# Kernel optimization log

Hardware: AMD Instinct MI355X
Metric: run time of the kernel (lower is better)

## Reference

```python
import jax, jax.numpy as jnp
import numpy as np

B, LATENT, P, NUM_ATOMS, H, L, E = 16, 128, 16, 64, 64, 4, 32768
N = P * NUM_ATOMS  # 1024

def _lin(k, i, o, s=0.05):
    kw, kb = jax.random.split(k)
    return jax.random.normal(kw, (i, o), jnp.float32) * s, jax.random.normal(kb, (o,), jnp.float32) * s

def setup_inputs() -> dict:
    key = jax.random.key(0)
    ks = jax.random.split(key, 32)
    z = jax.random.normal(ks[0], (B, LATENT), jnp.float32)
    edge_index = jax.random.randint(ks[1], (2, E), 0, N, jnp.int32)
    # build_node_features: (frame/P, atom/num_atoms, 1) per node
    fr = jnp.repeat(jnp.arange(P), NUM_ATOMS) / P
    at = jnp.tile(jnp.arange(NUM_ATOMS), P) / NUM_ATOMS
    node_features = jnp.stack([fr, at, jnp.ones(N)], -1).astype(jnp.float32)
    Wg, bg = _lin(ks[2], LATENT, H)
    Wn, bn = _lin(ks[3], 3, H)
    def stack(fn, base):
        outs = [fn(jax.random.fold_in(key, base + l)) for l in range(L)]
        return tuple(jnp.stack(t) for t in zip(*outs))
    eW1, eb1 = stack(lambda k: _lin(k, 2 * H + 1, H), 100)
    eW2, eb2 = stack(lambda k: _lin(k, H, H), 200)
    cW1, cb1 = stack(lambda k: _lin(k, H, H), 300)
    cW2 = jnp.stack([jax.random.normal(jax.random.fold_in(key, 400 + l), (H, 1), jnp.float32) * 0.05 for l in range(L)])
    nW1, nb1 = stack(lambda k: _lin(k, 2 * H, H), 500)
    nW2, nb2 = stack(lambda k: _lin(k, H, H), 600)
    lng = jnp.ones((L, H), jnp.float32)
    lnb = jnp.zeros((L, H), jnp.float32)
    oW1, ob1 = _lin(ks[4], H, H)
    oW2, ob2 = _lin(ks[5], H, 3)
    return dict(z=z, edge_index=edge_index, node_features=node_features, Wg=Wg, bg=bg, Wn=Wn, bn=bn,
                eW1=eW1, eb1=eb1, eW2=eW2, eb2=eb2, cW1=cW1, cb1=cb1, cW2=cW2,
                nW1=nW1, nb1=nb1, nW2=nW2, nb2=nb2, lng=lng, lnb=lnb,
                oW1=oW1, ob1=ob1, oW2=oW2, ob2=ob2)

def _forward(z, edge_index, node_features, Wg, bg, Wn, bn, eW1, eb1, eW2, eb2,
             cW1, cb1, cW2, nW1, nb1, nW2, nb2, lng, lnb, oW1, ob1, oW2, ob2):
    b = z.shape[0]
    n = node_features.shape[0]
    row, col = edge_index[0], edge_index[1]  # aggregate messages to row
    counts = jnp.clip(jnp.zeros((n,), jnp.float32).at[row].add(1.0), 1.0, None)
    g = z @ Wg + bg                              # [B,H]
    h = (node_features @ Wn + bn)[None] + g[:, None]  # [B,N,H]
    pos = jnp.zeros((b, n, 3), h.dtype)
    for l in range(L):
        hi, hj = h[:, row], h[:, col]            # [B,E,H] gathers
        diff = pos[:, row] - pos[:, col]         # [B,E,3]
        d2 = jnp.sum(diff * diff, -1, keepdims=True)
        m = jax.nn.silu(jnp.concatenate([hi, hj, d2], -1) @ eW1[l] + eb1[l])
        m = jax.nn.silu(m @ eW2[l] + eb2[l])     # [B,E,H]
        w = jax.nn.silu(m @ cW1[l] + cb1[l]) @ cW2[l]  # [B,E,1]
        trans = diff * w
        pos = pos + jnp.zeros_like(pos).at[:, row].add(trans) / counts[None, :, None]
        agg = jnp.zeros_like(h).at[:, row].add(m)      # scatter-sum to nodes
        u = jax.nn.silu(jnp.concatenate([h, agg], -1) @ nW1[l] + nb1[l]) @ nW2[l] + nb2[l]
        h = h + u                                 # node residual
        mu = jnp.mean(h, -1, keepdims=True)
        var = jnp.mean((h - mu) ** 2, -1, keepdims=True)
        h = (h - mu) * jax.lax.rsqrt(var + 1e-5) * lng[l] + lnb[l]
    out = jax.nn.relu(h @ oW1 + ob1) @ oW2 + ob2   # [B,N,3]
    return out.reshape(b, -1)

def reference(z, edge_index, node_features, Wg, bg, Wn, bn, eW1, eb1, eW2, eb2,
              cW1, cb1, cW2, nW1, nb1, nW2, nb2, lng, lnb, oW1, ob1, oW2, ob2):
    return _forward(z, edge_index, node_features, Wg, bg, Wn, bn, eW1, eb1, eW2, eb2,
                    cW1, cb1, cW2, nW1, nb1, nW2, nb2, lng, lnb, oW1, ob1, oW2, ob2)
```

## Files before the change

### kernel.cpp

```cpp
#include <hip/hip_runtime.h>
#include <hip/hip_bf16.h>


namespace {

constexpr int kB = 16, kN = 1024, kH = 64, kE = 32768, kLat = 128;
constexpr int kC = 24;
constexpr int kMaxItems = 2560;

typedef __attribute__((ext_vector_type(8))) short short8;
typedef __attribute__((ext_vector_type(4))) float floatx4;

__device__ __forceinline__ unsigned short f2bf(float f){
  union { float f; unsigned int u; } v; v.f = f;
  unsigned int r = v.u + 0x7fffu + ((v.u >> 16) & 1u);
  return (unsigned short)(r >> 16);
}
__device__ __forceinline__ unsigned int packbf(float a, float b){
  return ((unsigned int)f2bf(b) << 16) | (unsigned int)f2bf(a);
}
__device__ __forceinline__ unsigned int pack2f(float a, float b){
  unsigned int ua = __float_as_uint(a) + 0x8000u;
  unsigned int ub = __float_as_uint(b) + 0x8000u;
  return __builtin_amdgcn_perm(ub, ua, 0x07060302);
}
__device__ __forceinline__ float bflo(unsigned int u){
  union { unsigned int u; float f; } v; v.u = u << 16; return v.f;
}
__device__ __forceinline__ float bfhi(unsigned int u){
  union { unsigned int u; float f; } v; v.u = u & 0xffff0000u; return v.f;
}
__device__ __forceinline__ float silu2(float x){
  float u = __builtin_amdgcn_exp2f(-1.44269504f * x);
  return x * __builtin_amdgcn_rcpf(1.0f + u);
}

__global__ void k_count(const int* ei, int* cntI){
  int e = blockIdx.x*256 + threadIdx.x;
  atomicAdd(&cntI[ei[e]], 1);
}

__global__ void k_scan(const int* cntI, int* off, int* ioff, int* fill,
                       int* items, int* nitems){
  __shared__ int s0[1024];
  __shared__ int s1[1024];
  int t = threadIdx.x;
  int c = cntI[t];
  s0[t] = c; __syncthreads();
  int* src = s0; int* dst = s1;
  for (int o = 1; o < 1024; o <<= 1){
    int v = src[t] + ((t >= o) ? src[t-o] : 0);
    dst[t] = v; __syncthreads();
    int* tmp = src; src = dst; dst = tmp;
  }
  int inc = src[t];
  off[t] = inc - c;
  if (t == 1023) off[1024] = inc;
  fill[t] = 0;
  int ic = (c + (kC-1)) / kC;
  __syncthreads();
  s0[t] = ic; __syncthreads();
  src = s0; dst = s1;
  for (int o = 1; o < 1024; o <<= 1){
    int v = src[t] + ((t >= o) ? src[t-o] : 0);
    dst[t] = v; __syncthreads();
    int* tmp = src; src = dst; dst = tmp;
  }
  int inc2 = src[t];
  int ib = inc2 - ic;
  ioff[t] = ib;
  if (t == 1023){ ioff[1024] = inc2; *nitems = inc2; }
  for (int s = 0; s < ic; s++) items[ib + s] = (t << 12) | s;
}

__global__ void k_bucket(const int* ei, const int* off, int* fill, int* ecol,
                         const float* eW2, unsigned short* wfragE,
                         const float* z, const float* Wg, const float* bg,
                         float* g){
  int e = blockIdx.x*256 + threadIdx.x;
  int r = ei[e];
  int s = atomicAdd(&fill[r], 1);
  ecol[off[r] + s] = ei[kE + e];
  if (blockIdx.x < 4){
    int l = blockIdx.x;
    for (int i = threadIdx.x; i < 4096; i += 256){
      int f = i >> 9, lane = (i >> 3) & 63, j8 = i & 7;
      int jt = f >> 1, ks = f & 1;
      int k = ks*32 + (lane >> 4)*8 + j8;
      int j = jt*16 + (lane & 15);
      wfragE[l*4096 + i] = f2bf(eW2[l*4096 + k*64 + j]);
    }
  } else if (blockIdx.x < 8){
    int b = (blockIdx.x - 4)*4 + (threadIdx.x >> 6);
    int j = threadIdx.x & 63;
    float acc = bg[j];
    for (int k = 0; k < kLat; k++) acc += z[b*kLat + k] * Wg[k*64 + j];
    g[b*64 + j] = acc;
  }
}

__device__ __forceinline__ void stage16k(float* Wl, const float* src, int tid){
  const float4* p = (const float4*)src;
  float4* d = (float4*)Wl;
  d[tid]       = p[tid];
  d[tid + 256] = p[tid + 256];
  d[tid + 512] = p[tid + 512];
  d[tid + 768] = p[tid + 768];
}
__device__ __forceinline__ void xtwrite(float* XTl, int j0, int r0,
                                        const float v[4][4]){
  #pragma unroll
  for (int j = 0; j < 4; j++){
    float4 t = { v[0][j], v[1][j], v[2][j], v[3][j] };
    *(float4*)(XTl + (j0 + j)*68 + r0) = t;
  }
}
__device__ __forceinline__ void gemm64(const float* Wl, const float* XTl,
                                       int j0, int r0, float acc[4][4]){
  #pragma unroll 4
  for (int k = 0; k < 64; k++){
    float4 w = *(const float4*)(Wl + k*64 + j0);
    float4 x = *(const float4*)(XTl + k*68 + r0);
    float xv[4] = { x.x, x.y, x.z, x.w };
    float wv[4] = { w.x, w.y, w.z, w.w };
    #pragma unroll
    for (int i = 0; i < 4; i++)
      #pragma unroll
      for (int j = 0; j < 4; j++)
        acc[i][j] += xv[i]*wv[j];
  }
}

__global__ __launch_bounds__(256, 1) void k_preA(const float* nf, const float* Wn,
      const float* bn, const float* g, const float* eW1, const float* eb1,
      float* An1, float* An2, float* Ag1, float* Ag2){
  __shared__ __align__(16) float W0[4096];
  __shared__ __align__(16) float W1[4096];
  __shared__ __align__(16) float HR[16*68];
  int tid = threadIdx.x;
  if (blockIdx.x == 64){
    int bb = tid >> 4, j0 = (tid & 15)*4;
    float a1[4] = {0.f,0.f,0.f,0.f}, a2[4] = {0.f,0.f,0.f,0.f};
    for (int k = 0; k < 64; k++){
      float gk = g[bb*64 + k];
      float4 w1 = *(const float4*)(eW1 + k*64 + j0);
      float4 w2 = *(const float4*)(eW1 + 4096 + k*64 + j0);
      a1[0] += gk*w1.x; a1[1] += gk*w1.y; a1[2] += gk*w1.z; a1[3] += gk*w1.w;
      a2[0] += gk*w2.x; a2[1] += gk*w2.y; a2[2] += gk*w2.z; a2[3] += gk*w2.w;
    }
    float4 o1 = { a1[0], a1[1], a1[2], a1[3] };
    float4 o2 = { a2[0], a2[1], a2[2], a2[3] };
    *(float4*)(Ag1 + bb*64 + j0) = o1;
    *(float4*)(Ag2 + bb*64 + j0) = o2;
    return;
  }
  {
    const float4* e1a = (const float4*)(eW1);
    const float4* e1b = (const float4*)(eW1 + 4096);
    for (int i = tid; i < 1024; i += 256){
      ((float4*)W0)[i] = e1a[i]; ((float4*)W1)[i] = e1b[i];
    }
  }
  int rl = tid >> 4, c = tid & 15, j0 = c*4;
  int n = blockIdx.x*16 + rl;
  float f0 = nf[n*3], f1 = nf[n*3+1], f2 = nf[n*3+2];
  float4 hv;
  hv.x = f0*Wn[j0+0] + f1*Wn[64+j0+0] + f2*Wn[128+j0+0] + bn[j0+0];
  hv.y = f0*Wn[j0+1] + f1*Wn[64+j0+1] + f2*Wn[128+j0+1] + bn[j0+1];
  hv.z = f0*Wn[j0+2] + f1*Wn[64+j0+2] + f2*Wn[128+j0+2] + bn[j0+2];
  hv.w = f0*Wn[j0+3] + f1*Wn[64+j0+3] + f2*Wn[128+j0+3] + bn[j0+3];
  *(float4*)(HR + rl*68 + j0) = hv;
  __syncthreads();
  float4 b1 = *(const float4*)(eb1 + j0);
  float a1[4] = { b1.x, b1.y, b1.z, b1.w };
  float a2[4] = { 0.f, 0.f, 0.f, 0.f };
  #pragma unroll 8
  for (int k = 0; k < 64; k++){
    float hk = HR[rl*68 + k];
    float4 w1 = *(const float4*)(W0 + k*64 + j0);
    float4 w2 = *(const float4*)(W1 + k*64 + j0);
    a1[0] += hk*w1.x; a1[1] += hk*w1.y; a1[2] += hk*w1.z; a1[3] += hk*w1.w;
    a2[0] += hk*w2.x; a2[1] += hk*w2.y; a2[2] += hk*w2.z; a2[3] += hk*w2.w;
  }
  float4 o1 = { a1[0], a1[1], a1[2], a1[3] };
  float4 o2 = { a2[0], a2[1], a2[2], a2[3] };
  *(float4*)(An1 + n*64 + j0) = o1;
  *(float4*)(An2 + n*64 + j0) = o2;
}

__global__ __launch_bounds__(256, 1) void k_pre1(const float* nf, const float* Wn,
      const float* bn, const float* g, const float* An1, const float* An2,
      const float* Ag1, const float* Ag2, float* h, float* A1t,
      unsigned short* A2bf){
  int idx = blockIdx.x*256 + threadIdx.x;
  int row = idx >> 4;
  int j0  = (idx & 15) * 4;
  int n = row >> 4, bb = row & 15;
  float4 a1 = *(const float4*)(An1 + n*64 + j0);
  float4 g1 = *(const float4*)(Ag1 + bb*64 + j0);
  a1.x += g1.x; a1.y += g1.y; a1.z += g1.z; a1.w += g1.w;
  *(float4*)(A1t + row*64 + j0) = a1;
  float4 a2 = *(const float4*)(An2 + n*64 + j0);
  float4 g2 = *(const float4*)(Ag2 + bb*64 + j0);
  a2.x += g2.x; a2.y += g2.y; a2.z += g2.z; a2.w += g2.w;
  uint2 pk; pk.x = packbf(a2.x, a2.y); pk.y = packbf(a2.z, a2.w);
  *(uint2*)(A2bf + row*64 + j0) = pk;
  float f0 = nf[n*3], f1 = nf[n*3+1], f2 = nf[n*3+2];
  float4 w0 = *(const float4*)(Wn + j0);
  float4 w1 = *(const float4*)(Wn + 64 + j0);
  float4 w2 = *(const float4*)(Wn + 128 + j0);
  float4 bv = *(const float4*)(bn + j0);
  float4 gv = *(const float4*)(g + bb*64 + j0);
  float4 hv;
  hv.x = f0*w0.x + f1*w1.x + f2*w2.x + bv.x + gv.x;
  hv.y = f0*w0.y + f1*w1.y + f2*w2.y + bv.y + gv.y;
  hv.z = f0*w0.z + f1*w1.z + f2*w2.z + bv.z + gv.z;
  hv.w = f0*w0.w + f1*w1.w + f2*w2.w + bv.w + gv.w;
  *(float4*)(h + (bb*1024 + n)*64 + j0) = hv;
}

__global__ __launch_bounds__(256, 3) void k_edge(const float* A1t,
      const unsigned short* A2bf, const unsigned short* wfragE,
      const float* eb2, int l, const int* off, const int* ecol,
      const int* items, const int* nitems, float* P){
  int w = blockIdx.x*4 + (threadIdx.x >> 6);
  if (w >= *nitems) return;
  int lane = threadIdx.x & 63;
  int m = lane & 15, quad = lane >> 4;
  int it = items[w];
  int r = it >> 12, s = it & 4095;
  int e0 = off[r] + s*kC;
  int e1 = min(off[r+1], e0 + kC);

  short8 wf[8];
  #pragma unroll
  for (int f = 0; f < 8; f++)
    wf[f] = *(const short8*)(wfragE + l*4096 + f*512 + lane*8);

  float4 a1[4];
  #pragma unroll
  for (int ks = 0; ks < 2; ks++){
    a1[ks*2+0] = *(const float4*)(A1t + (r<<10) + (m<<6) + ks*32 + quad*8);
    a1[ks*2+1] = *(const float4*)(A1t + (r<<10) + (m<<6) + ks*32 + quad*8 + 4);
  }
  floatx4 dini[4];
  #pragma unroll
  for (int jt = 0; jt < 4; jt++)
    dini[jt] = *(const floatx4*)(eb2 + l*64 + jt*16 + quad*4);
  floatx4 agg[4];
  #pragma unroll
  for (int jt = 0; jt < 4; jt++) agg[jt] = (floatx4){0.f,0.f,0.f,0.f};

  int c0 = ecol[e0];
  uint4 p0 = *(const uint4*)(A2bf + ((c0<<4)+m)*64 + quad*8);
  uint4 p1 = *(const uint4*)(A2bf + ((c0<<4)+m)*64 + 32 + quad*8);

  for (int e = e0; e < e1; e++){
    uint4 c_0 = p0, c_1 = p1;
    if (e + 1 < e1){
      int cn = ecol[e+1];
      p0 = *(const uint4*)(A2bf + ((cn<<4)+m)*64 + quad*8);
      p1 = *(const uint4*)(A2bf + ((cn<<4)+m)*64 + 32 + quad*8);
    }
    short8 bfr[2];
    #pragma unroll
    for (int ks = 0; ks < 2; ks++){
      uint4 a2r = (ks == 0) ? c_0 : c_1;
      float4 x0 = a1[ks*2+0];
      float4 x1 = a1[ks*2+1];
      float v0 = silu2(x0.x + bflo(a2r.x));
      float v1 = silu2(x0.y + bfhi(a2r.x));
      float v2 = silu2(x0.z + bflo(a2r.y));
      float v3 = silu2(x0.w + bfhi(a2r.y));
      float v4 = silu2(x1.x + bflo(a2r.z));
      float v5 = silu2(x1.y + bfhi(a2r.z));
      float v6 = silu2(x1.z + bflo(a2r.w));
      float v7 = silu2(x1.w + bfhi(a2r.w));
      union { uint4 u; short8 s; } bu;
      bu.u.x = pack2f(v0, v1); bu.u.y = pack2f(v2, v3);
      bu.u.z = pack2f(v4, v5); bu.u.w = pack2f(v6, v7);
      bfr[ks] = bu.s;
    }
    #pragma unroll
    for (int jt = 0; jt < 4; jt++){
      floatx4 d = dini[jt];
      d = __builtin_amdgcn_mfma_f32_16x16x32_bf16(wf[jt*2+0], bfr[0], d, 0, 0, 0);
      d = __builtin_amdgcn_mfma_f32_16x16x32_bf16(wf[jt*2+1], bfr[1], d, 0, 0, 0);
      floatx4 a = agg[jt];
      a.x += silu2(d.x); a.y += silu2(d.y);
      a.z += silu2(d.z); a.w += silu2(d.w);
      agg[jt] = a;
    }
  }
  #pragma unroll
  for (int jt = 0; jt < 4; jt++)
    *(floatx4*)(P + w*1024 + m*64 + jt*16 + quad*4) = agg[jt];
}

template <bool LAST>
__global__ __launch_bounds__(256, 1) void k_post(int l, float* h, const float* P,
      const int* ioff, const float* nW1, const float* nb1_, const float* nW2,
      const float* nb2_, const float* lng_, const float* lnb_,
      const float* eW1, const float* eb1_, float* A1t, unsigned short* A2bf,
      const float* oW1, const float* ob1_, const float* oW2, const float* ob2_,
      float* out){
  __shared__ __align__(16) float W[4096];
  __shared__ __align__(16) float XT[64*68];
  int tid = threadIdx.x;
  int bb = blockIdx.x >> 4;
  int n0 = (blockIdx.x & 15) * 64;
  int c = tid & 15, g = tid >> 4;
  int j0 = c*4, r0 = g*4;
  int rowbase = bb*1024 + n0 + r0;

  stage16k(W, nW1 + l*8192, tid);
  float hold[4][4];
  #pragma unroll
  for (int i = 0; i < 4; i++){
    float4 v = *(const float4*)(h + (rowbase + i)*64 + j0);
    hold[i][0]=v.x; hold[i][1]=v.y; hold[i][2]=v.z; hold[i][3]=v.w;
  }
  xtwrite(XT, j0, r0, hold);
  float acc[4][4];
  {
    float4 b1 = *(const float4*)(nb1_ + l*64 + j0);
    float bv[4] = { b1.x, b1.y, b1.z, b1.w };
    #pragma unroll
    for (int i = 0; i < 4; i++)
      #pragma unroll
      for (int j = 0; j < 4; j++) acc[i][j] = bv[j];
  }
  __syncthreads();
  gemm64(W, XT, j0, r0, acc);
  __syncthreads();

  stage16k(W, nW1 + l*8192 + 4096, tid);
  {
    float agt[4][4];
    #pragma unroll
    for (int i = 0; i < 4; i++){
      int n = n0 + r0 + i;
      float4 s = { 0.f, 0.f, 0.f, 0.f };
      int i0 = ioff[n], i1 = ioff[n+1];
      for (int it = i0; it < i1; it++){
        float4 v = *(const float4*)(P + it*1024 + bb*64 + j0);
        s.x += v.x; s.y += v.y; s.z += v.z; s.w += v.w;
      }
      agt[i][0]=s.x; agt[i][1]=s.y; agt[i][2]=s.z; agt[i][3]=s.w;
    }
    xtwrite(XT, j0, r0, agt);
  }
  __syncthreads();
  gemm64(W, XT, j0, r0, acc);
  #pragma unroll
  for (int i = 0; i < 4; i++)
    #pragma unroll
    for (int j = 0; j < 4; j++) acc[i][j] = silu2(acc[i][j]);
  __syncthreads();

  stage16k(W, nW2 + l*4096, tid);
  xtwrite(XT, j0, r0, acc);
  float u[4][4];
  {
    float4 b2 = *(const float4*)(nb2_ + l*64 + j0);
    float bv[4] = { b2.x, b2.y, b2.z, b2.w };
    #pragma unroll
    for (int i = 0; i < 4; i++)
      #pragma unroll
      for (int j = 0; j < 4; j++) u[i][j] = bv[j];
  }
  __syncthreads();
  gemm64(W, XT, j0, r0, u);
  float4 lgv = *(const float4*)(lng_ + l*64 + j0);
  float4 lbv = *(const float4*)(lnb_ + l*64 + j0);
  float hn[4][4];
  #pragma unroll
  for (int i = 0; i < 4; i++){
    float hv[4];
    #pragma unroll
    for (int j = 0; j < 4; j++) hv[j] = hold[i][j] + u[i][j];
    float s1 = hv[0]+hv[1]+hv[2]+hv[3];
    float s2 = hv[0]*hv[0]+hv[1]*hv[1]+hv[2]*hv[2]+hv[3]*hv[3];
    s1 += __shfl_xor(s1, 1, 64); s1 += __shfl_xor(s1, 2, 64);
    s1 += __shfl_xor(s1, 4, 64); s1 += __shfl_xor(s1, 8, 64);
    s2 += __shfl_xor(s2, 1, 64); s2 += __shfl_xor(s2, 2, 64);
    s2 += __shfl_xor(s2, 4, 64); s2 += __shfl_xor(s2, 8, 64);
    float mu  = s1 * (1.0f/64.0f);
    float var = s2 * (1.0f/64.0f) - mu*mu;
    float rs  = rsqrtf(var + 1e-5f);
    hn[i][0] = (hv[0]-mu)*rs*lgv.x + lbv.x;
    hn[i][1] = (hv[1]-mu)*rs*lgv.y + lbv.y;
    hn[i][2] = (hv[2]-mu)*rs*lgv.z + lbv.z;
    hn[i][3] = (hv[3]-mu)*rs*lgv.w + lbv.w;
  }

  if (!LAST){
    #pragma unroll
    for (int i = 0; i < 4; i++){
      float4 v = { hn[i][0], hn[i][1], hn[i][2], hn[i][3] };
      *(float4*)(h + (rowbase + i)*64 + j0) = v;
    }
    __syncthreads();
    stage16k(W, eW1 + (l+1)*8256, tid);
    xtwrite(XT, j0, r0, hn);
    float a1[4][4];
    {
      float4 b1 = *(const float4*)(eb1_ + (l+1)*64 + j0);
      float bv[4] = { b1.x, b1.y, b1.z, b1.w };
      #pragma unroll
      for (int i = 0; i < 4; i++)
        #pragma unroll
        for (int j = 0; j < 4; j++) a1[i][j] = bv[j];
    }
    __syncthreads();
    gemm64(W, XT, j0, r0, a1);
    __syncthreads();
    stage16k(W, eW1 + (l+1)*8256 + 4096, tid);
    float a2[4][4];
    #pragma unroll
    for (int i = 0; i < 4; i++)
      #pragma unroll
      for (int j = 0; j < 4; j++) a2[i][j] = 0.f;
    __syncthreads();
    gemm64(W, XT, j0, r0, a2);
    #pragma unroll
    for (int i = 0; i < 4; i++){
      int tb = ((n0 + r0 + i)*16 + bb)*64 + j0;
      float4 o1 = { a1[i][0], a1[i][1], a1[i][2], a1[i][3] };
      *(float4*)(A1t + tb) = o1;
      uint2 pk; pk.x = packbf(a2[i][0], a2[i][1]);
      pk.y = packbf(a2[i][2], a2[i][3]);
      *(uint2*)(A2bf + tb) = pk;
    }
  } else {
    __syncthreads();
    stage16k(W, oW1, tid);
    xtwrite(XT, j0, r0, hn);
    float tr[4][4];
    {
      float4 b1 = *(const float4*)(ob1_ + j0);
      float bv[4] = { b1.x, b1.y, b1.z, b1.w };
      #pragma unroll
      for (int i = 0; i < 4; i++)
        #pragma unroll
        for (int j = 0; j < 4; j++) tr[i][j] = bv[j];
    }
    __syncthreads();
    gemm64(W, XT, j0, r0, tr);
    #pragma unroll
    for (int i = 0; i < 4; i++)
      #pragma unroll
      for (int j = 0; j < 4; j++) tr[i][j] = fmaxf(tr[i][j], 0.f);
    float po[4][3];
    #pragma unroll
    for (int i = 0; i < 4; i++){ po[i][0]=0.f; po[i][1]=0.f; po[i][2]=0.f; }
    #pragma unroll
    for (int j = 0; j < 4; j++){
      float w0 = oW2[(j0+j)*3 + 0];
      float w1 = oW2[(j0+j)*3 + 1];
      float w2 = oW2[(j0+j)*3 + 2];
      #pragma unroll
      for (int i = 0; i < 4; i++){
        po[i][0] += tr[i][j]*w0;
        po[i][1] += tr[i][j]*w1;
        po[i][2] += tr[i][j]*w2;
      }
    }
    #pragma unroll
    for (int i = 0; i < 4; i++)
      #pragma unroll
      for (int uu = 0; uu < 3; uu++){
        float v = po[i][uu];
        v += __shfl_xor(v, 1, 64); v += __shfl_xor(v, 2, 64);
        v += __shfl_xor(v, 4, 64); v += __shfl_xor(v, 8, 64);
        po[i][uu] = v;
      }
    if (c == 0){
      #pragma unroll
      for (int i = 0; i < 4; i++){
        int n = n0 + r0 + i;
        out[bb*3072 + n*3 + 0] = po[i][0] + ob2_[0];
        out[bb*3072 + n*3 + 1] = po[i][1] + ob2_[1];
        out[bb*3072 + n*3 + 2] = po[i][2] + ob2_[2];
      }
    }
  }
}

}

extern "C" void kernel_launch(void* const* d_in, const int* in_sizes, int n_in,
                              void* d_out, int out_size, void* d_ws, size_t ws_size,
                              hipStream_t stream){
  const float* z   = (const float*)d_in[0];
  const int*   ei  = (const int*)d_in[1];
  const float* nf  = (const float*)d_in[2];
  const float* Wg  = (const float*)d_in[3];  const float* bg  = (const float*)d_in[4];
  const float* Wn  = (const float*)d_in[5];  const float* bn  = (const float*)d_in[6];
  const float* eW1 = (const float*)d_in[7];  const float* eb1 = (const float*)d_in[8];
  const float* eW2 = (const float*)d_in[9];  const float* eb2 = (const float*)d_in[10];
  const float* nW1 = (const float*)d_in[14]; const float* nb1 = (const float*)d_in[15];
  const float* nW2 = (const float*)d_in[16]; const float* nb2 = (const float*)d_in[17];
  const float* lng = (const float*)d_in[18]; const float* lnb = (const float*)d_in[19];
  const float* oW1 = (const float*)d_in[20]; const float* ob1 = (const float*)d_in[21];
  const float* oW2 = (const float*)d_in[22]; const float* ob2 = (const float*)d_in[23];

  float* W      = (float*)d_ws;
  float* h      = W;
  float* A1t    = W + 1048576;
  unsigned short* A2bf   = (unsigned short*)(W + 2097152);
  unsigned short* wfragE = (unsigned short*)(W + 2621440);
  float* P      = W + 2629632;
  float* g      = W + 5251072;
  int*   cntI   = (int*)(W + 5252096);
  int*   off    = cntI + 1024;
  int*   ioff   = off + 1025;
  int*   fill   = ioff + 1025;
  int*   items  = fill + 1024;
  int*   nitems = items + 2560;
  int*   ecol   = nitems + 1;
  float* An1    = W + 5291776;
  float* An2    = An1 + 65536;
  float* Ag1    = An2 + 65536;
  float* Ag2    = Ag1 + 1024;

  hipMemsetAsync(cntI, 0, 1024*sizeof(int), stream);
  k_count <<<128, 256, 0, stream>>>(ei, cntI);
  k_scan  <<<1,  1024, 0, stream>>>(cntI, off, ioff, fill, items, nitems);
  k_bucket<<<128, 256, 0, stream>>>(ei, off, fill, ecol, eW2, wfragE, z, Wg, bg, g);
  k_preA  <<<65,  256, 0, stream>>>(nf, Wn, bn, g, eW1, eb1, An1, An2, Ag1, Ag2);
  k_pre1  <<<1024,256, 0, stream>>>(nf, Wn, bn, g, An1, An2, Ag1, Ag2, h, A1t, A2bf);

  for (int l = 0; l < 4; l++){
    k_edge<<<640, 256, 0, stream>>>(A1t, A2bf, wfragE, eb2, l, off, ecol,
                                    items, nitems, P);
    if (l < 3)
      k_post<false><<<256, 256, 0, stream>>>(l, h, P, ioff, nW1, nb1, nW2, nb2,
            lng, lnb, eW1, eb1, A1t, A2bf, oW1, ob1, oW2, ob2, (float*)d_out);
    else
      k_post<true> <<<256, 256, 0, stream>>>(l, h, P, ioff, nW1, nb1, nW2, nb2,
            lng, lnb, eW1, eb1, A1t, A2bf, oW1, ob1, oW2, ob2, (float*)d_out);
  }
}
```

Baseline: 356.7 us.

## Fuse edge message pass into per-node layer kernel with ping-pong buffers

```diff
diff --git a/kernel.cpp b/kernel.cpp
--- a/kernel.cpp
+++ b/kernel.cpp
@@ -4,9 +4,7 @@
 
 namespace {
 
-constexpr int kB = 16, kN = 1024, kH = 64, kE = 32768, kLat = 128;
-constexpr int kC = 24;
-constexpr int kMaxItems = 2560;
+constexpr int kE = 32768, kLat = 128;
 
 typedef __attribute__((ext_vector_type(8))) short short8;
 typedef __attribute__((ext_vector_type(4))) float floatx4;
@@ -35,18 +33,48 @@
   return x * __builtin_amdgcn_rcpf(1.0f + u);
 }
 
-__global__ void k_count(const int* ei, int* cntI){
-  int e = blockIdx.x*256 + threadIdx.x;
-  atomicAdd(&cntI[ei[e]], 1);
-}
-
-__global__ void k_scan(const int* cntI, int* off, int* ioff, int* fill,
-                       int* items, int* nitems){
+__device__ __forceinline__ void stage16k(float* Wl, const float* src, int tid){
+  const float4* p = (const float4*)src;
+  float4* d = (float4*)Wl;
+  d[tid]       = p[tid];
+  d[tid + 256] = p[tid + 256];
+  d[tid + 512] = p[tid + 512];
+  d[tid + 768] = p[tid + 768];
+}
+__device__ __forceinline__ void xtwrite(float* XTl, int j0, int r0,
+                                        const float v[4][4]){
+  #pragma unroll
+  for (int j = 0; j < 4; j++){
+    float4 t = { v[0][j], v[1][j], v[2][j], v[3][j] };
+    *(float4*)(XTl + (j0 + j)*68 + r0) = t;
+  }
+}
+__device__ __forceinline__ void gemm64(const float* Wl, const float* XTl,
+                                       int j0, int r0, float acc[4][4]){
+  #pragma unroll 4
+  for (int k = 0; k < 64; k++){
+    float4 w = *(const float4*)(Wl + k*64 + j0);
+    float4 x = *(const float4*)(XTl + k*68 + r0);
+    float xv[4] = { x.x, x.y, x.z, x.w };
+    float wv[4] = { w.x, w.y, w.z, w.w };
+    #pragma unroll
+    for (int i = 0; i < 4; i++)
+      #pragma unroll
+      for (int j = 0; j < 4; j++)
+        acc[i][j] += xv[i]*wv[j];
+  }
+}
+
+__global__ void k_scancnt(const int* ei, int* off, int* fill){
   __shared__ int s0[1024];
   __shared__ int s1[1024];
   int t = threadIdx.x;
-  int c = cntI[t];
-  s0[t] = c; __syncthreads();
+  s0[t] = 0; fill[t] = 0;
+  __syncthreads();
+  #pragma unroll
+  for (int i = 0; i < 32; i++) atomicAdd(&s0[ei[i*1024 + t]], 1);
+  __syncthreads();
+  int c = s0[t];
   int* src = s0; int* dst = s1;
   for (int o = 1; o < 1024; o <<= 1){
     int v = src[t] + ((t >= o) ? src[t-o] : 0);
@@ -56,21 +84,6 @@
   int inc = src[t];
   off[t] = inc - c;
   if (t == 1023) off[1024] = inc;
-  fill[t] = 0;
-  int ic = (c + (kC-1)) / kC;
-  __syncthreads();
-  s0[t] = ic; __syncthreads();
-  src = s0; dst = s1;
-  for (int o = 1; o < 1024; o <<= 1){
-    int v = src[t] + ((t >= o) ? src[t-o] : 0);
-    dst[t] = v; __syncthreads();
-    int* tmp = src; src = dst; dst = tmp;
-  }
-  int inc2 = src[t];
-  int ib = inc2 - ic;
-  ioff[t] = ib;
-  if (t == 1023){ ioff[1024] = inc2; *nitems = inc2; }
-  for (int s = 0; s < ic; s++) items[ib + s] = (t << 12) | s;
 }
 
 __global__ void k_bucket(const int* ei, const int* off, int* fill, int* ecol,
@@ -99,38 +112,6 @@
   }
 }
 
-__device__ __forceinline__ void stage16k(float* Wl, const float* src, int tid){
-  const float4* p = (const float4*)src;
-  float4* d = (float4*)Wl;
-  d[tid]       = p[tid];
-  d[tid + 256] = p[tid + 256];
-  d[tid + 512] = p[tid + 512];
-  d[tid + 768] = p[tid + 768];
-}
-__device__ __forceinline__ void xtwrite(float* XTl, int j0, int r0,
-                                        const float v[4][4]){
-  #pragma unroll
-  for (int j = 0; j < 4; j++){
-    float4 t = { v[0][j], v[1][j], v[2][j], v[3][j] };
-    *(float4*)(XTl + (j0 + j)*68 + r0) = t;
-  }
-}
-__device__ __forceinline__ void gemm64(const float* Wl, const float* XTl,
-                                       int j0, int r0, float acc[4][4]){
-  #pragma unroll 4
-  for (int k = 0; k < 64; k++){
-    float4 w = *(const float4*)(Wl + k*64 + j0);
-    float4 x = *(const float4*)(XTl + k*68 + r0);
-    float xv[4] = { x.x, x.y, x.z, x.w };
-    float wv[4] = { w.x, w.y, w.z, w.w };
-    #pragma unroll
-    for (int i = 0; i < 4; i++)
-      #pragma unroll
-      for (int j = 0; j < 4; j++)
-        acc[i][j] += xv[i]*wv[j];
-  }
-}
-
 __global__ __launch_bounds__(256, 1) void k_preA(const float* nf, const float* Wn,
       const float* bn, const float* g, const float* eW1, const float* eb1,
       float* An1, float* An2, float* Ag1, float* Ag2){
@@ -190,8 +171,8 @@
 
 __global__ __launch_bounds__(256, 1) void k_pre1(const float* nf, const float* Wn,
       const float* bn, const float* g, const float* An1, const float* An2,
-      const float* Ag1, const float* Ag2, float* h, float* A1t,
-      unsigned short* A2bf){
+      const float* Ag1, const float* Ag2, float* h, float* A1,
+      unsigned short* A2){
   int idx = blockIdx.x*256 + threadIdx.x;
   int row = idx >> 4;
   int j0  = (idx & 15) * 4;
@@ -199,12 +180,12 @@
   float4 a1 = *(const float4*)(An1 + n*64 + j0);
   float4 g1 = *(const float4*)(Ag1 + bb*64 + j0);
   a1.x += g1.x; a1.y += g1.y; a1.z += g1.z; a1.w += g1.w;
-  *(float4*)(A1t + row*64 + j0) = a1;
+  *(float4*)(A1 + row*64 + j0) = a1;
   float4 a2 = *(const float4*)(An2 + n*64 + j0);
   float4 g2 = *(const float4*)(Ag2 + bb*64 + j0);
   a2.x += g2.x; a2.y += g2.y; a2.z += g2.z; a2.w += g2.w;
   uint2 pk; pk.x = packbf(a2.x, a2.y); pk.y = packbf(a2.z, a2.w);
-  *(uint2*)(A2bf + row*64 + j0) = pk;
+  *(uint2*)(A2 + row*64 + j0) = pk;
   float f0 = nf[n*3], f1 = nf[n*3+1], f2 = nf[n*3+2];
   float4 w0 = *(const float4*)(Wn + j0);
   float4 w1 = *(const float4*)(Wn + 64 + j0);
@@ -219,156 +200,134 @@
   *(float4*)(h + (bb*1024 + n)*64 + j0) = hv;
 }
 
-__global__ __launch_bounds__(256, 3) void k_edge(const float* A1t,
-      const unsigned short* A2bf, const unsigned short* wfragE,
-      const float* eb2, int l, const int* off, const int* ecol,
-      const int* items, const int* nitems, float* P){
-  int w = blockIdx.x*4 + (threadIdx.x >> 6);
-  if (w >= *nitems) return;
-  int lane = threadIdx.x & 63;
-  int m = lane & 15, quad = lane >> 4;
-  int it = items[w];
-  int r = it >> 12, s = it & 4095;
-  int e0 = off[r] + s*kC;
-  int e1 = min(off[r+1], e0 + kC);
-
-  short8 wf[8];
-  #pragma unroll
-  for (int f = 0; f < 8; f++)
-    wf[f] = *(const short8*)(wfragE + l*4096 + f*512 + lane*8);
-
-  float4 a1[4];
-  #pragma unroll
-  for (int ks = 0; ks < 2; ks++){
-    a1[ks*2+0] = *(const float4*)(A1t + (r<<10) + (m<<6) + ks*32 + quad*8);
-    a1[ks*2+1] = *(const float4*)(A1t + (r<<10) + (m<<6) + ks*32 + quad*8 + 4);
-  }
-  floatx4 dini[4];
-  #pragma unroll
-  for (int jt = 0; jt < 4; jt++)
-    dini[jt] = *(const floatx4*)(eb2 + l*64 + jt*16 + quad*4);
-  floatx4 agg[4];
-  #pragma unroll
-  for (int jt = 0; jt < 4; jt++) agg[jt] = (floatx4){0.f,0.f,0.f,0.f};
-
-  int c0 = ecol[e0];
-  uint4 p0 = *(const uint4*)(A2bf + ((c0<<4)+m)*64 + quad*8);
-  uint4 p1 = *(const uint4*)(A2bf + ((c0<<4)+m)*64 + 32 + quad*8);
-
-  for (int e = e0; e < e1; e++){
-    uint4 c_0 = p0, c_1 = p1;
-    if (e + 1 < e1){
-      int cn = ecol[e+1];
-      p0 = *(const uint4*)(A2bf + ((cn<<4)+m)*64 + quad*8);
-      p1 = *(const uint4*)(A2bf + ((cn<<4)+m)*64 + 32 + quad*8);
-    }
-    short8 bfr[2];
-    #pragma unroll
-    for (int ks = 0; ks < 2; ks++){
-      uint4 a2r = (ks == 0) ? c_0 : c_1;
-      float4 x0 = a1[ks*2+0];
-      float4 x1 = a1[ks*2+1];
-      float v0 = silu2(x0.x + bflo(a2r.x));
-      float v1 = silu2(x0.y + bfhi(a2r.x));
-      float v2 = silu2(x0.z + bflo(a2r.y));
-      float v3 = silu2(x0.w + bfhi(a2r.y));
-      float v4 = silu2(x1.x + bflo(a2r.z));
-      float v5 = silu2(x1.y + bfhi(a2r.z));
-      float v6 = silu2(x1.z + bflo(a2r.w));
-      float v7 = silu2(x1.w + bfhi(a2r.w));
-      union { uint4 u; short8 s; } bu;
-      bu.u.x = pack2f(v0, v1); bu.u.y = pack2f(v2, v3);
-      bu.u.z = pack2f(v4, v5); bu.u.w = pack2f(v6, v7);
-      bfr[ks] = bu.s;
-    }
-    #pragma unroll
-    for (int jt = 0; jt < 4; jt++){
-      floatx4 d = dini[jt];
-      d = __builtin_amdgcn_mfma_f32_16x16x32_bf16(wf[jt*2+0], bfr[0], d, 0, 0, 0);
-      d = __builtin_amdgcn_mfma_f32_16x16x32_bf16(wf[jt*2+1], bfr[1], d, 0, 0, 0);
-      floatx4 a = agg[jt];
-      a.x += silu2(d.x); a.y += silu2(d.y);
-      a.z += silu2(d.z); a.w += silu2(d.w);
-      agg[jt] = a;
-    }
-  }
-  #pragma unroll
-  for (int jt = 0; jt < 4; jt++)
-    *(floatx4*)(P + w*1024 + m*64 + jt*16 + quad*4) = agg[jt];
-}
-
 template <bool LAST>
-__global__ __launch_bounds__(256, 1) void k_post(int l, float* h, const float* P,
-      const int* ioff, const float* nW1, const float* nb1_, const float* nW2,
-      const float* nb2_, const float* lng_, const float* lnb_,
-      const float* eW1, const float* eb1_, float* A1t, unsigned short* A2bf,
+__global__ __launch_bounds__(256) void k_layer(int l,
+      const float* A1r, const unsigned short* A2r,
+      float* A1w, unsigned short* A2w,
+      float* h, const unsigned short* wfragE, const float* eb2,
+      const int* off, const int* ecol,
+      const float* nW1, const float* nb1_, const float* nW2, const float* nb2_,
+      const float* lng_, const float* lnb_, const float* eW1, const float* eb1_,
       const float* oW1, const float* ob1_, const float* oW2, const float* ob2_,
       float* out){
   __shared__ __align__(16) float W[4096];
   __shared__ __align__(16) float XT[64*68];
-  int tid = threadIdx.x;
-  int bb = blockIdx.x >> 4;
-  int n0 = (blockIdx.x & 15) * 64;
-  int c = tid & 15, g = tid >> 4;
-  int j0 = c*4, r0 = g*4;
-  int rowbase = bb*1024 + n0 + r0;
+  __shared__ __align__(16) float AGL[64*68];
+  __shared__ float W2o[192];
+  __shared__ float ob2s[4];
+  int tid = threadIdx.x, bid = blockIdx.x;
+  int n0 = bid * 4;
+  int lane = tid & 63, wv = tid >> 6, m = lane & 15, quad = lane >> 4;
+
+  {
+    int nd = n0 + wv;
+    short8 wf[8];
+    #pragma unroll
+    for (int f = 0; f < 8; f++)
+      wf[f] = *(const short8*)(wfragE + l*4096 + f*512 + lane*8);
+    floatx4 dini[4], agg[4];
+    #pragma unroll
+    for (int jt = 0; jt < 4; jt++){
+      dini[jt] = *(const floatx4*)(eb2 + l*64 + jt*16 + quad*4);
+      agg[jt] = (floatx4){0.f,0.f,0.f,0.f};
+    }
+    int e0 = off[nd], e1 = off[nd+1];
+    if (e0 < e1){
+      float4 a1[4];
+      #pragma unroll
+      for (int ks = 0; ks < 2; ks++){
+        a1[ks*2+0] = *(const float4*)(A1r + (nd<<10) + (m<<6) + ks*32 + quad*8);
+        a1[ks*2+1] = *(const float4*)(A1r + (nd<<10) + (m<<6) + ks*32 + quad*8 + 4);
+      }
+      int c0 = ecol[e0];
+      uint4 p0 = *(const uint4*)(A2r + ((c0<<4)+m)*64 + quad*8);
+      uint4 p1 = *(const uint4*)(A2r + ((c0<<4)+m)*64 + 32 + quad*8);
+      for (int e = e0; e < e1; e++){
+        uint4 c_0 = p0, c_1 = p1;
+        if (e + 1 < e1){
+          int cn = ecol[e+1];
+          p0 = *(const uint4*)(A2r + ((cn<<4)+m)*64 + quad*8);
+          p1 = *(const uint4*)(A2r + ((cn<<4)+m)*64 + 32 + quad*8);
+        }
+        short8 bfr[2];
+        #pragma unroll
+        for (int ks = 0; ks < 2; ks++){
+          uint4 a2r = (ks == 0) ? c_0 : c_1;
+          float4 x0 = a1[ks*2+0];
+          float4 x1 = a1[ks*2+1];
+          float v0 = silu2(x0.x + bflo(a2r.x));
+          float v1 = silu2(x0.y + bfhi(a2r.x));
+          float v2 = silu2(x0.z + bflo(a2r.y));
+          float v3 = silu2(x0.w + bfhi(a2r.y));
+          float v4 = silu2(x1.x + bflo(a2r.z));
+          float v5 = silu2(x1.y + bfhi(a2r.z));
+          float v6 = silu2(x1.z + bflo(a2r.w));
+          float v7 = silu2(x1.w + bfhi(a2r.w));
+          union { uint4 u; short8 s; } bu;
+          bu.u.x = pack2f(v0, v1); bu.u.y = pack2f(v2, v3);
+          bu.u.z = pack2f(v4, v5); bu.u.w = pack2f(v6, v7);
+          bfr[ks] = bu.s;
+        }
+        #pragma unroll
+        for (int jt = 0; jt < 4; jt++){
+          floatx4 d = dini[jt];
+          d = __builtin_amdgcn_mfma_f32_16x16x32_bf16(wf[jt*2+0], bfr[0], d, 0, 0, 0);
+          d = __builtin_amdgcn_mfma_f32_16x16x32_bf16(wf[jt*2+1], bfr[1], d, 0, 0, 0);
+          floatx4 a = agg[jt];
+          a.x += silu2(d.x); a.y += silu2(d.y);
+          a.z += silu2(d.z); a.w += silu2(d.w);
+          agg[jt] = a;
+        }
+      }
+    }
+    #pragma unroll
+    for (int jt = 0; jt < 4; jt++){
+      #pragma unroll
+      for (int i = 0; i < 4; i++)
+        AGL[(jt*16 + quad*4 + i)*68 + wv*16 + m] = agg[jt][i];
+    }
+  }
+
+  int c = tid & 15, gq = tid >> 4;
+  int j0 = c*4, r0 = gq*4;
 
   stage16k(W, nW1 + l*8192, tid);
   float hold[4][4];
   #pragma unroll
   for (int i = 0; i < 4; i++){
-    float4 v = *(const float4*)(h + (rowbase + i)*64 + j0);
+    int rr = r0 + i;
+    int n = n0 + (rr >> 4), bb = rr & 15;
+    float4 v = *(const float4*)(h + (bb*1024 + n)*64 + j0);
     hold[i][0]=v.x; hold[i][1]=v.y; hold[i][2]=v.z; hold[i][3]=v.w;
   }
   xtwrite(XT, j0, r0, hold);
   float acc[4][4];
-  {
-    float4 b1 = *(const float4*)(nb1_ + l*64 + j0);
+  { float4 b1 = *(const float4*)(nb1_ + l*64 + j0);
     float bv[4] = { b1.x, b1.y, b1.z, b1.w };
     #pragma unroll
     for (int i = 0; i < 4; i++)
       #pragma unroll
-      for (int j = 0; j < 4; j++) acc[i][j] = bv[j];
-  }
+      for (int j = 0; j < 4; j++) acc[i][j] = bv[j]; }
   __syncthreads();
   gemm64(W, XT, j0, r0, acc);
   __syncthreads();
-
   stage16k(W, nW1 + l*8192 + 4096, tid);
-  {
-    float agt[4][4];
-    #pragma unroll
-    for (int i = 0; i < 4; i++){
-      int n = n0 + r0 + i;
-      float4 s = { 0.f, 0.f, 0.f, 0.f };
-      int i0 = ioff[n], i1 = ioff[n+1];
-      for (int it = i0; it < i1; it++){
-        float4 v = *(const float4*)(P + it*1024 + bb*64 + j0);
-        s.x += v.x; s.y += v.y; s.z += v.z; s.w += v.w;
-      }
-      agt[i][0]=s.x; agt[i][1]=s.y; agt[i][2]=s.z; agt[i][3]=s.w;
-    }
-    xtwrite(XT, j0, r0, agt);
-  }
-  __syncthreads();
-  gemm64(W, XT, j0, r0, acc);
+  __syncthreads();
+  gemm64(W, AGL, j0, r0, acc);
   #pragma unroll
   for (int i = 0; i < 4; i++)
     #pragma unroll
     for (int j = 0; j < 4; j++) acc[i][j] = silu2(acc[i][j]);
   __syncthreads();
-
   stage16k(W, nW2 + l*4096, tid);
   xtwrite(XT, j0, r0, acc);
   float u[4][4];
-  {
-    float4 b2 = *(const float4*)(nb2_ + l*64 + j0);
+  { float4 b2 = *(const float4*)(nb2_ + l*64 + j0);
     float bv[4] = { b2.x, b2.y, b2.z, b2.w };
     #pragma unroll
     for (int i = 0; i < 4; i++)
       #pragma unroll
-      for (int j = 0; j < 4; j++) u[i][j] = bv[j];
-  }
+      for (int j = 0; j < 4; j++) u[i][j] = bv[j]; }
   __syncthreads();
   gemm64(W, XT, j0, r0, u);
   float4 lgv = *(const float4*)(lng_ + l*64 + j0);
@@ -397,55 +356,57 @@
   if (!LAST){
     #pragma unroll
     for (int i = 0; i < 4; i++){
+      int rr = r0 + i;
+      int n = n0 + (rr >> 4), bb = rr & 15;
       float4 v = { hn[i][0], hn[i][1], hn[i][2], hn[i][3] };
-      *(float4*)(h + (rowbase + i)*64 + j0) = v;
+      *(float4*)(h + (bb*1024 + n)*64 + j0) = v;
     }
     __syncthreads();
     stage16k(W, eW1 + (l+1)*8256, tid);
     xtwrite(XT, j0, r0, hn);
-    float a1[4][4];
-    {
-      float4 b1 = *(const float4*)(eb1_ + (l+1)*64 + j0);
+    float a1r[4][4];
+    { float4 b1 = *(const float4*)(eb1_ + (l+1)*64 + j0);
       float bv[4] = { b1.x, b1.y, b1.z, b1.w };
       #pragma unroll
       for (int i = 0; i < 4; i++)
         #pragma unroll
-        for (int j = 0; j < 4; j++) a1[i][j] = bv[j];
-    }
+        for (int j = 0; j < 4; j++) a1r[i][j] = bv[j]; }
     __syncthreads();
-    gemm64(W, XT, j0, r0, a1);
+    gemm64(W, XT, j0, r0, a1r);
     __syncthreads();
     stage16k(W, eW1 + (l+1)*8256 + 4096, tid);
-    float a2[4][4];
+    float a2r[4][4];
     #pragma unroll
     for (int i = 0; i < 4; i++)
       #pragma unroll
-      for (int j = 0; j < 4; j++) a2[i][j] = 0.f;
+      for (int j = 0; j < 4; j++) a2r[i][j] = 0.f;
     __syncthreads();
-    gemm64(W, XT, j0, r0, a2);
+    gemm64(W, XT, j0, r0, a2r);
     #pragma unroll
     for (int i = 0; i < 4; i++){
-      int tb = ((n0 + r0 + i)*16 + bb)*64 + j0;
-      float4 o1 = { a1[i][0], a1[i][1], a1[i][2], a1[i][3] };
-      *(float4*)(A1t + tb) = o1;
-      uint2 pk; pk.x = packbf(a2[i][0], a2[i][1]);
-      pk.y = packbf(a2[i][2], a2[i][3]);
-      *(uint2*)(A2bf + tb) = pk;
+      int rr = r0 + i;
+      int n = n0 + (rr >> 4), bb = rr & 15;
+      int tb = (n*16 + bb)*64 + j0;
+      float4 o1 = { a1r[i][0], a1r[i][1], a1r[i][2], a1r[i][3] };
+      *(float4*)(A1w + tb) = o1;
+      uint2 pk; pk.x = packbf(a2r[i][0], a2r[i][1]);
+      pk.y = packbf(a2r[i][2], a2r[i][3]);
+      *(uint2*)(A2w + tb) = pk;
     }
   } else {
     __syncthreads();
     stage16k(W, oW1, tid);
+    if (tid < 192) W2o[tid] = oW2[tid];
+    if (tid < 3)   ob2s[tid] = ob2_[tid];
     xtwrite(XT, j0, r0, hn);
+    __syncthreads();
     float tr[4][4];
-    {
-      float4 b1 = *(const float4*)(ob1_ + j0);
+    { float4 b1 = *(const float4*)(ob1_ + j0);
       float bv[4] = { b1.x, b1.y, b1.z, b1.w };
       #pragma unroll
       for (int i = 0; i < 4; i++)
         #pragma unroll
-        for (int j = 0; j < 4; j++) tr[i][j] = bv[j];
-    }
-    __syncthreads();
+        for (int j = 0; j < 4; j++) tr[i][j] = bv[j]; }
     gemm64(W, XT, j0, r0, tr);
     #pragma unroll
     for (int i = 0; i < 4; i++)
@@ -456,9 +417,9 @@
     for (int i = 0; i < 4; i++){ po[i][0]=0.f; po[i][1]=0.f; po[i][2]=0.f; }
     #pragma unroll
     for (int j = 0; j < 4; j++){
-      float w0 = oW2[(j0+j)*3 + 0];
-      float w1 = oW2[(j0+j)*3 + 1];
-      float w2 = oW2[(j0+j)*3 + 2];
+      float w0 = W2o[(j0+j)*3 + 0];
+      float w1 = W2o[(j0+j)*3 + 1];
+      float w2 = W2o[(j0+j)*3 + 2];
       #pragma unroll
       for (int i = 0; i < 4; i++){
         po[i][0] += tr[i][j]*w0;
@@ -478,10 +439,11 @@
     if (c == 0){
       #pragma unroll
       for (int i = 0; i < 4; i++){
-        int n = n0 + r0 + i;
-        out[bb*3072 + n*3 + 0] = po[i][0] + ob2_[0];
-        out[bb*3072 + n*3 + 1] = po[i][1] + ob2_[1];
-        out[bb*3072 + n*3 + 2] = po[i][2] + ob2_[2];
+        int rr = r0 + i;
+        int n = n0 + (rr >> 4), bb = rr & 15;
+        out[bb*3072 + n*3 + 0] = po[i][0] + ob2s[0];
+        out[bb*3072 + n*3 + 1] = po[i][1] + ob2s[1];
+        out[bb*3072 + n*3 + 2] = po[i][2] + ob2s[2];
       }
     }
   }
@@ -507,38 +469,37 @@
 
   float* W      = (float*)d_ws;
   float* h      = W;
-  float* A1t    = W + 1048576;
-  unsigned short* A2bf   = (unsigned short*)(W + 2097152);
-  unsigned short* wfragE = (unsigned short*)(W + 2621440);
-  float* P      = W + 2629632;
-  float* g      = W + 5251072;
-  int*   cntI   = (int*)(W + 5252096);
-  int*   off    = cntI + 1024;
-  int*   ioff   = off + 1025;
-  int*   fill   = ioff + 1025;
-  int*   items  = fill + 1024;
-  int*   nitems = items + 2560;
-  int*   ecol   = nitems + 1;
-  float* An1    = W + 5291776;
-  float* An2    = An1 + 65536;
-  float* Ag1    = An2 + 65536;
-  float* Ag2    = Ag1 + 1024;
-
-  hipMemsetAsync(cntI, 0, 1024*sizeof(int), stream);
-  k_count <<<128, 256, 0, stream>>>(ei, cntI);
-  k_scan  <<<1,  1024, 0, stream>>>(cntI, off, ioff, fill, items, nitems);
-  k_bucket<<<128, 256, 0, stream>>>(ei, off, fill, ecol, eW2, wfragE, z, Wg, bg, g);
-  k_preA  <<<65,  256, 0, stream>>>(nf, Wn, bn, g, eW1, eb1, An1, An2, Ag1, Ag2);
-  k_pre1  <<<1024,256, 0, stream>>>(nf, Wn, bn, g, An1, An2, Ag1, Ag2, h, A1t, A2bf);
+  float* A1a    = W + 1048576;
+  float* A1b    = W + 2097152;
+  unsigned short* A2a    = (unsigned short*)(W + 3145728);
+  unsigned short* A2b    = (unsigned short*)(W + 3670016);
+  unsigned short* wfragE = (unsigned short*)(W + 4194304);
+  float* g      = W + 4202496;
+  float* An1    = W + 4203520;
+  float* An2    = W + 4269056;
+  float* Ag1    = W + 4334592;
+  float* Ag2    = W + 4335616;
+  int*   off    = (int*)(W + 4336640);
+  int*   fill   = off + 1025;
+  int*   ecol   = fill + 1024;
+
+  k_scancnt<<<1, 1024, 0, stream>>>(ei, off, fill);
+  k_bucket <<<128, 256, 0, stream>>>(ei, off, fill, ecol, eW2, wfragE, z, Wg, bg, g);
+  k_preA   <<<65,  256, 0, stream>>>(nf, Wn, bn, g, eW1, eb1, An1, An2, Ag1, Ag2);
+  k_pre1   <<<1024,256, 0, stream>>>(nf, Wn, bn, g, An1, An2, Ag1, Ag2, h, A1a, A2a);
 
   for (int l = 0; l < 4; l++){
-    k_edge<<<640, 256, 0, stream>>>(A1t, A2bf, wfragE, eb2, l, off, ecol,
-                                    items, nitems, P);
+    const float* A1r = (l & 1) ? A1b : A1a;
+    const unsigned short* A2r = (l & 1) ? A2b : A2a;
+    float* A1w = (l & 1) ? A1a : A1b;
+    unsigned short* A2w = (l & 1) ? A2a : A2b;
     if (l < 3)
-      k_post<false><<<256, 256, 0, stream>>>(l, h, P, ioff, nW1, nb1, nW2, nb2,
-            lng, lnb, eW1, eb1, A1t, A2bf, oW1, ob1, oW2, ob2, (float*)d_out);
+      k_layer<false><<<256, 256, 0, stream>>>(l, A1r, A2r, A1w, A2w, h, wfragE,
+            eb2, off, ecol, nW1, nb1, nW2, nb2, lng, lnb, eW1, eb1,
+            oW1, ob1, oW2, ob2, (float*)d_out);
     else
-      k_post<true> <<<256, 256, 0, stream>>>(l, h, P, ioff, nW1, nb1, nW2, nb2,
-            lng, lnb, eW1, eb1, A1t, A2bf, oW1, ob1, oW2, ob2, (float*)d_out);
-  }
-}
+      k_layer<true> <<<256, 256, 0, stream>>>(l, A1r, A2r, A1w, A2w, h, wfragE,
+            eb2, off, ecol, nW1, nb1, nW2, nb2, lng, lnb, eW1, eb1,
+            oW1, ob1, oW2, ob2, (float*)d_out);
+  }
+}
```

New measurement: 336.2 us. -5.7%, faster.
